# Optimization experiments

Hardware: AMD Instinct MI355X
Metric: run time of the kernel (lower is better)

The kernel has to match this reference:

```python
import jax, jax.numpy as jnp
import numpy as np

INPUT_DIM = 512
LATENT_DIM = 64
H1, H2 = 128, 64  # hardcoded hidden widths in Encoder/Decoder
BATCH = 4096


def _xavier(key, shape):
    fan_out, fan_in = shape
    std = jnp.sqrt(2.0 / (fan_in + fan_out))
    return std * jax.random.normal(key, shape, dtype=jnp.float32)


def setup_inputs() -> dict:
    key = jax.random.key(0)
    ks = jax.random.split(key, 10)
    d = LATENT_DIM
    n_pairs = d * (d - 1) // 2
    n_funcs = 1 + d + n_pairs  # bias + states + pairwise products
    inp = {
        "x": jax.random.normal(ks[0], (BATCH, INPUT_DIM), dtype=jnp.float32),
        "xdot": jax.random.normal(ks[1], (BATCH, INPUT_DIM), dtype=jnp.float32),
        # encoder weights (torch Linear layout: [out, in])
        "We1": _xavier(ks[2], (H1, INPUT_DIM)), "be1": jnp.zeros((H1,), jnp.float32),
        "We2": _xavier(ks[3], (H2, H1)),        "be2": jnp.zeros((H2,), jnp.float32),
        "We3": _xavier(ks[4], (d, H2)),         "be3": jnp.zeros((d,), jnp.float32),
        # decoder weights
        "Wd1": _xavier(ks[5], (H2, d)),         "bd1": jnp.zeros((H2,), jnp.float32),
        "Wd2": _xavier(ks[6], (H1, H2)),        "bd2": jnp.zeros((H1,), jnp.float32),
        "Wd3": _xavier(ks[7], (INPUT_DIM, H1)), "bd3": jnp.zeros((INPUT_DIM,), jnp.float32),
        "XI": jnp.ones((n_funcs, d), jnp.float32),
        "XI_mask": jnp.ones((n_funcs, d), jnp.float32),
    }
    return inp


def _mlp_with_jacobian(x, Ws, bs):
    """3-layer relu MLP; returns output and per-sample analytic Jacobian [B,out,in].
    Jacobian = diag(m3) W3 diag(m2) W2 diag(m1) W1 with relu masks m_l."""
    h = x
    J = None
    for W, b in zip(Ws, bs):
        h = h @ W.T + b                      # [B, out_l]
        m = (h > 0).astype(h.dtype)          # relu mask (grad 0 at 0, matching torch)
        h = jnp.maximum(h, 0)
        Wm = m[:, :, None] * W[None]         # [B, out_l, in_l]
        J = Wm if J is None else jnp.einsum('boh,bhi->boi', Wm, J)
    return h, J


def _sindy_library(z):
    B, d = z.shape
    iu, ju = np.triu_indices(d, k=1)
    ones = jnp.ones((B, 1), z.dtype)
    pairs = z[:, iu] * z[:, ju]              # [B, d(d-1)/2]
    return jnp.concatenate([ones, z, pairs], axis=1)


def reference(x, xdot, We1, be1, We2, be2, We3, be3,
              Wd1, bd1, Wd2, bd2, Wd3, bd3, XI, XI_mask):
    z, Jenc = _mlp_with_jacobian(x, (We1, We2, We3), (be1, be2, be3))
    dz_dt = jnp.einsum('bli,bi->bl', Jenc, xdot)
    xh, Jdec = _mlp_with_jacobian(z, (Wd1, Wd2, Wd3), (bd1, bd2, bd3))
    theta = _sindy_library(z)
    dz_dt_sindy = theta @ (XI_mask * XI)
    dxh_dt = jnp.einsum('bol,bl->bo', Jdec, dz_dt_sindy)
    return (xh, dxh_dt, z, dz_dt, dz_dt_sindy)
```

## Files before the change

kernel.cpp:

```cpp
#include <hip/hip_runtime.h>

#define BATCH 4096
#define IN_DIM 512
#define H1DIM 128
#define H2DIM 64
#define DDIM 64
#define NFUNC 2081
#define NFPAD 2112
#define CHUNK 704
#define KS_PER_CHUNK 22

typedef short bf16x8 __attribute__((ext_vector_type(8)));
typedef float f32x4 __attribute__((ext_vector_type(4)));
#define MFMA(a,b,c) __builtin_amdgcn_mfma_f32_16x16x32_bf16(a,b,c,0,0,0)

#define WSZ1 (H1DIM*IN_DIM)
#define WSZ2 (H2DIM*H1DIM)
#define WSZ3 (DDIM*H2DIM)
#define WSZ4 (H2DIM*DDIM)
#define WSZ5 (H1DIM*H2DIM)
#define WSZ6 (IN_DIM*H1DIM)

__device__ __forceinline__ short f2b(float f) {
    union { float f; unsigned u; } x; x.f = f;
    unsigned r = x.u + 0x7fffu + ((x.u >> 16) & 1u);
    return (short)(r >> 16);
}
__device__ __forceinline__ float b2f(short s) {
    union { unsigned u; float f; } x; x.u = ((unsigned)(unsigned short)s) << 16;
    return x.f;
}
__device__ __forceinline__ void split3f(float v, short& s0, short& s1, short& s2) {
    s0 = f2b(v); float r = v - b2f(s0);
    s1 = f2b(r); float r2 = r - b2f(s1);
    s2 = f2b(r2);
}
__device__ __forceinline__ uint2 pk4(const short* s) {
    union { short s[4]; uint2 u; } z;
    z.s[0] = s[0]; z.s[1] = s[1]; z.s[2] = s[2]; z.s[3] = s[3];
    return z.u;
}

__device__ __forceinline__ void st_b16(short* t, int RS, int r, int c, short v) {
    int b = (c * 2) ^ ((r & 7) << 4);
    *(short*)((char*)(t + r * RS) + b) = v;
}
__device__ __forceinline__ void st_b64(short* t, int RS, int r, int c0, uint2 v) {
    int b = (c0 * 2) ^ ((r & 7) << 4);
    *(uint2*)((char*)(t + r * RS) + b) = v;
}
__device__ __forceinline__ bf16x8 ld_af(const short* t, int RS, int lane, int kbase) {
    int r = lane & 15;
    int b = ((kbase + (lane >> 4) * 8) * 2) ^ ((r & 7) << 4);
    return *(const bf16x8*)((const char*)(t + r * RS) + b);
}
__device__ __forceinline__ bf16x8 ld_bp(const short* P, int blk, int lane) {
    return *(const bf16x8*)(P + ((size_t)blk * 64 + lane) * 8);
}

__device__ __forceinline__ void mf9(bf16x8 f0, bf16x8 f1, bf16x8 f2, bf16x8 fv,
                                    bf16x8 b0, bf16x8 b1, bf16x8 b2,
                                    f32x4& P, f32x4& Q, f32x4& V) {
    P = MFMA(f0, b0, P); Q = MFMA(f1, b1, Q);
    P = MFMA(f1, b0, P); Q = MFMA(f0, b1, Q);
    P = MFMA(f2, b0, P); Q = MFMA(f2, b1, Q);
    P = MFMA(f0, b2, P); Q = MFMA(f1, b2, Q);
    V = MFMA(fv, b0, V);
}

__device__ __forceinline__ void epi_store(short* t0, short* t1, short* t2, short* tv, int RS,
                                          int lane, int col, const f32x4& P, const f32x4& Q,
                                          const f32x4& V, float bb)
{
    #pragma unroll
    for (int q = 0; q < 4; ++q) {
        int row = (lane >> 4) * 4 + q;
        float pre = P[q] + Q[q] + bb;
        float h = fmaxf(pre, 0.f);
        short s0, s1, s2;
        split3f(h, s0, s1, s2);
        st_b16(t0, RS, row, col, s0);
        st_b16(t1, RS, row, col, s1);
        st_b16(t2, RS, row, col, s2);
        st_b16(tv, RS, row, col, pre > 0.f ? f2b(V[q]) : (short)0);
    }
}

template<int K>
__device__ void pack_w(const float* __restrict__ W, short* __restrict__ dst, int NK,
                       int gid, int nthr)
{
    for (int i = gid; i < NK; i += nthr) {
        int c = i / K, k = i % K;
        int cb = c >> 4, ks = k >> 5;
        int L = (((k >> 3) & 3) << 4) | (c & 15);
        int j = k & 7;
        int idx = ((cb * (K / 32) + ks) * 64 + L) * 8 + j;
        short s0, s1, s2; split3f(W[i], s0, s1, s2);
        dst[idx] = s0; dst[idx + NK] = s1; dst[idx + 2 * NK] = s2;
    }
}

__global__ void initk(const float* __restrict__ x, const float* __restrict__ xdot,
                      const float* __restrict__ We1, const float* __restrict__ We2,
                      const float* __restrict__ We3, const float* __restrict__ Wd1,
                      const float* __restrict__ Wd2, const float* __restrict__ Wd3,
                      const float* __restrict__ XI, const float* __restrict__ XIm,
                      float* __restrict__ xh, float* __restrict__ dxh,
                      short* Wp1, short* Wp2, short* Wp3, short* Wp4, short* Wp5, short* Wp6,
                      short* xiP, int2* pk)
{
    int gid = blockIdx.x * blockDim.x + threadIdx.x;
    int nthr = gridDim.x * blockDim.x;

    for (int i = gid; i < (BATCH / 16) * 16 * 64; i += nthr) {
        int L = i & 63, ks = (i >> 6) & 15, rb = i >> 10;
        int row = rb * 16 + (L & 15);
        int k0 = ks * 32 + ((L >> 4) << 3);
        const float* px = &x[(size_t)row * IN_DIM + k0];
        const float* pd = &xdot[(size_t)row * IN_DIM + k0];
        union { short s[8]; bf16x8 v; } a0, a1, a2, dv;
        #pragma unroll
        for (int j = 0; j < 8; ++j) {
            split3f(px[j], a0.s[j], a1.s[j], a2.s[j]);
            dv.s[j] = f2b(pd[j]);
        }
        short* bx = (short*)(xh + (size_t)rb * 8192);
        short* bd = (short*)(dxh + (size_t)rb * 8192);
        int off = (ks * 64 + L) * 8;
        *(bf16x8*)(bx + off) = a0.v;
        *(bf16x8*)(bx + 8192 + off) = a1.v;
        *(bf16x8*)(bd + off) = a2.v;
        *(bf16x8*)(bd + 8192 + off) = dv.v;
    }

    pack_w<512>(We1, Wp1, WSZ1, gid, nthr);
    pack_w<128>(We2, Wp2, WSZ2, gid, nthr);
    pack_w<64>(We3, Wp3, WSZ3, gid, nthr);
    pack_w<64>(Wd1, Wp4, WSZ4, gid, nthr);
    pack_w<64>(Wd2, Wp5, WSZ5, gid, nthr);
    pack_w<128>(Wd3, Wp6, WSZ6, gid, nthr);

    for (int i = gid; i < 4 * 66 * 64; i += nthr) {
        int cb = i / (66 * 64);
        int r = i - cb * (66 * 64);
        int ks = r >> 6, L = r & 63;
        int col = cb * 16 + (L & 15);
        union { short s[8]; bf16x8 v; } w;
        #pragma unroll
        for (int j = 0; j < 8; ++j) {
            int f = ks * 32 + ((L >> 4) << 3) + j;
            float v = (f < NFUNC) ? XI[(size_t)f * DDIM + col] * XIm[(size_t)f * DDIM + col] : 0.f;
            w.s[j] = f2b(v);
        }
        *(bf16x8*)(xiP + (size_t)i * 8) = w.v;
    }

    for (int f = gid; f < NFPAD; f += nthr) {
        int a, b;
        if (f == 0) { a = 64; b = 64; }
        else if (f <= DDIM) { a = f - 1; b = 64; }
        else if (f < NFUNC) {
            int p = f - 1 - DDIM; int i2 = 0, cum = 0;
            while (cum + (63 - i2) <= p) { cum += 63 - i2; ++i2; }
            a = i2; b = i2 + 1 + (p - cum);
        } else { a = 65; b = 65; }
        pk[f] = make_int2(a, b);
    }
}

__global__ __launch_bounds__(256, 1)
void fused(const float* __restrict__ be1, const float* __restrict__ be2,
           const float* __restrict__ be3, const float* __restrict__ bd1,
           const float* __restrict__ bd2, const float* __restrict__ bd3,
           const short* __restrict__ Wp1, const short* __restrict__ Wp2,
           const short* __restrict__ Wp3, const short* __restrict__ Wp4,
           const short* __restrict__ Wp5, const short* __restrict__ Wp6,
           const short* __restrict__ xiP, const int2* __restrict__ pk,
           float* __restrict__ xh, float* __restrict__ dxh, float* __restrict__ zo,
           float* __restrict__ dz, float* __restrict__ dzs)
{
    __shared__ __align__(16) char ldsbuf[37120];
    short* h1s0 = (short*)(ldsbuf + 0);
    short* h1s1 = (short*)(ldsbuf + 4096);
    short* h1s2 = (short*)(ldsbuf + 8192);
    short* v1   = (short*)(ldsbuf + 12288);
    short* h2s0 = (short*)(ldsbuf + 16384);
    short* h2s1 = (short*)(ldsbuf + 18432);
    short* h2s2 = (short*)(ldsbuf + 20480);
    short* v2   = (short*)(ldsbuf + 22528);
    short* th   = (short*)(ldsbuf + 0);
    short* g1s0 = (short*)(ldsbuf + 0);
    short* g1s1 = (short*)(ldsbuf + 2048);
    short* g1s2 = (short*)(ldsbuf + 4096);
    short* u1   = (short*)(ldsbuf + 6144);
    short* g2s0 = (short*)(ldsbuf + 8192);
    short* g2s1 = (short*)(ldsbuf + 12288);
    short* g2s2 = (short*)(ldsbuf + 16384);
    short* u2   = (short*)(ldsbuf + 20480);
    short* zb0  = (short*)(ldsbuf + 24576);
    short* zb1  = (short*)(ldsbuf + 26624);
    short* zb2  = (short*)(ldsbuf + 28672);
    short* dzsb = (short*)(ldsbuf + 30720);
    float* zf   = (float*)(ldsbuf + 32768);

    const int tid = threadIdx.x, lane = tid & 63, wave = tid >> 6;
    const int row0 = blockIdx.x * 16;
    const int c16 = lane & 15;

    float bb1[2] = { be1[wave * 32 + c16], be1[wave * 32 + 16 + c16] };
    float bb2 = be2[wave * 16 + c16];
    float bb3 = be3[wave * 16 + c16];
    float bD1 = bd1[wave * 16 + c16];
    float bD2[2] = { bd2[wave * 32 + c16], bd2[wave * 32 + 16 + c16] };
    float bD3[8];
    #pragma unroll
    for (int i = 0; i < 8; ++i) bD3[i] = bd3[wave * 128 + i * 16 + c16];

    bf16x8 L2B[4][3];

    {
        const short* bx = (const short*)(xh + (size_t)blockIdx.x * 8192);
        const short* bd = (const short*)(dxh + (size_t)blockIdx.x * 8192);
        f32x4 P[2] = {}, Q[2] = {}, V[2] = {};
        bf16x8 A0[3], A1[3], A2[3], Ad[3];
        bf16x8 B0[3][2], B1[3][2], B2[3][2];
#define L1_LA(ks, sl) { int off = ((ks) * 64 + lane) * 8; \
        A0[sl] = *(const bf16x8*)(bx + off); A1[sl] = *(const bf16x8*)(bx + 8192 + off); \
        A2[sl] = *(const bf16x8*)(bd + off); Ad[sl] = *(const bf16x8*)(bd + 8192 + off); }
#define L1_LB(ks, sl) { int bA = (wave * 2) * 16 + (ks), bB = (wave * 2 + 1) * 16 + (ks); \
        B0[sl][0] = ld_bp(Wp1, bA, lane); B1[sl][0] = ld_bp(Wp1 + WSZ1, bA, lane); B2[sl][0] = ld_bp(Wp1 + 2 * WSZ1, bA, lane); \
        B0[sl][1] = ld_bp(Wp1, bB, lane); B1[sl][1] = ld_bp(Wp1 + WSZ1, bB, lane); B2[sl][1] = ld_bp(Wp1 + 2 * WSZ1, bB, lane); }
        L1_LA(0, 0) L1_LB(0, 0)
        L1_LA(1, 1) L1_LB(1, 1)
        L1_LA(2, 2) L1_LB(2, 2)
        #pragma unroll
        for (int ks = 0; ks < 16; ++ks) {
            const int sl = ks % 3;
            mf9(A0[sl], A1[sl], A2[sl], Ad[sl], B0[sl][0], B1[sl][0], B2[sl][0], P[0], Q[0], V[0]);
            mf9(A0[sl], A1[sl], A2[sl], Ad[sl], B0[sl][1], B1[sl][1], B2[sl][1], P[1], Q[1], V[1]);
            if (ks + 3 < 16) { L1_LA(ks + 3, sl) L1_LB(ks + 3, sl) }
        }
#undef L1_LA
#undef L1_LB
        #pragma unroll
        for (int nf = 0; nf < 2; ++nf) {
            int col = wave * 32 + nf * 16 + c16;
            epi_store(h1s0, h1s1, h1s2, v1, 128, lane, col, P[nf], Q[nf], V[nf], bb1[nf]);
        }
        #pragma unroll
        for (int ks = 0; ks < 4; ++ks) {
            int blk = wave * 4 + ks;
            L2B[ks][0] = ld_bp(Wp2, blk, lane);
            L2B[ks][1] = ld_bp(Wp2 + WSZ2, blk, lane);
            L2B[ks][2] = ld_bp(Wp2 + 2 * WSZ2, blk, lane);
        }
    }
    __syncthreads();

    bf16x8 L3B[2][3];
    {
        bf16x8 Aa[4][4];
        #pragma unroll
        for (int ks = 0; ks < 4; ++ks) {
            Aa[ks][0] = ld_af(h1s0, 128, lane, ks * 32);
            Aa[ks][1] = ld_af(h1s1, 128, lane, ks * 32);
            Aa[ks][2] = ld_af(h1s2, 128, lane, ks * 32);
            Aa[ks][3] = ld_af(v1, 128, lane, ks * 32);
        }
        f32x4 P = {}, Q = {}, V = {};
        #pragma unroll
        for (int ks = 0; ks < 4; ++ks)
            mf9(Aa[ks][0], Aa[ks][1], Aa[ks][2], Aa[ks][3], L2B[ks][0], L2B[ks][1], L2B[ks][2], P, Q, V);
        epi_store(h2s0, h2s1, h2s2, v2, 64, lane, wave * 16 + c16, P, Q, V, bb2);
        #pragma unroll
        for (int ks = 0; ks < 2; ++ks) {
            int blk = wave * 2 + ks;
            L3B[ks][0] = ld_bp(Wp3, blk, lane);
            L3B[ks][1] = ld_bp(Wp3 + WSZ3, blk, lane);
            L3B[ks][2] = ld_bp(Wp3 + 2 * WSZ3, blk, lane);
        }
    }
    __syncthreads();

    {
        bf16x8 Aa[2][4];
        #pragma unroll
        for (int ks = 0; ks < 2; ++ks) {
            Aa[ks][0] = ld_af(h2s0, 64, lane, ks * 32);
            Aa[ks][1] = ld_af(h2s1, 64, lane, ks * 32);
            Aa[ks][2] = ld_af(h2s2, 64, lane, ks * 32);
            Aa[ks][3] = ld_af(v2, 64, lane, ks * 32);
        }
        f32x4 P = {}, Q = {}, V = {};
        #pragma unroll
        for (int ks = 0; ks < 2; ++ks)
            mf9(Aa[ks][0], Aa[ks][1], Aa[ks][2], Aa[ks][3], L3B[ks][0], L3B[ks][1], L3B[ks][2], P, Q, V);
        int col = wave * 16 + c16;
        #pragma unroll
        for (int q = 0; q < 4; ++q) {
            int row = (lane >> 4) * 4 + q;
            float pre = P[q] + Q[q] + bb3;
            float hz = fmaxf(pre, 0.f);
            float vz = pre > 0.f ? V[q] : 0.f;
            zf[row * 68 + col] = hz;
            short s0, s1, s2;
            split3f(hz, s0, s1, s2);
            st_b16(zb0, 64, row, col, s0);
            st_b16(zb1, 64, row, col, s1);
            st_b16(zb2, 64, row, col, s2);
            zo[(size_t)(row0 + row) * DDIM + col] = hz;
            dz[(size_t)(row0 + row) * DDIM + col] = vz;
        }
        if (tid < 32) { int r = tid & 15; zf[r * 68 + 64 + (tid >> 4)] = (tid >> 4) ? 0.f : 1.f; }
    }
    __syncthreads();

    {
        f32x4 sa0 = {}, sa1 = {};
        const int tr = tid & 15, tf44 = (tid >> 4) * 44;
        bf16x8 X[KS_PER_CHUNK];
        #pragma unroll
        for (int kk = 0; kk < KS_PER_CHUNK; ++kk)
            X[kk] = ld_bp(xiP, wave * 66 + kk, lane);
        #pragma unroll
        for (int ch = 0; ch < 3; ++ch) {
            #pragma unroll
            for (int g = 0; g < 11; ++g) {
                int fl = tf44 + g * 4;
                int fg = ch * CHUNK + fl;
                int4 qa = *(const int4*)&pk[fg];
                int4 qb = *(const int4*)&pk[fg + 2];
                float t0 = zf[tr * 68 + qa.x] * zf[tr * 68 + qa.y];
                float t1 = zf[tr * 68 + qa.z] * zf[tr * 68 + qa.w];
                float t2 = zf[tr * 68 + qb.x] * zf[tr * 68 + qb.y];
                float t3 = zf[tr * 68 + qb.z] * zf[tr * 68 + qb.w];
                short arr[4] = { f2b(t0), f2b(t1), f2b(t2), f2b(t3) };
                st_b64(th, 704, tr, fl, pk4(arr));
            }
            __syncthreads();
            #pragma unroll
            for (int kk = 0; kk < KS_PER_CHUNK; ++kk) {
                bf16x8 a = ld_af(th, 704, lane, kk * 32);
                if (kk & 1) sa1 = MFMA(a, X[kk], sa1);
                else        sa0 = MFMA(a, X[kk], sa0);
            }
            if (ch < 2) {
                #pragma unroll
                for (int kk = 0; kk < KS_PER_CHUNK; ++kk)
                    X[kk] = ld_bp(xiP, wave * 66 + (ch + 1) * KS_PER_CHUNK + kk, lane);
            }
            __syncthreads();
        }
        f32x4 sacc = sa0 + sa1;
        int col = wave * 16 + c16;
        #pragma unroll
        for (int q = 0; q < 4; ++q) {
            int row = (lane >> 4) * 4 + q;
            float v = sacc[q];
            dzs[(size_t)(row0 + row) * DDIM + col] = v;
            st_b16(dzsb, 64, row, col, f2b(v));
        }
    }
    bf16x8 D1B[2][3];
    #pragma unroll
    for (int ks = 0; ks < 2; ++ks) {
        int blk = wave * 2 + ks;
        D1B[ks][0] = ld_bp(Wp4, blk, lane);
        D1B[ks][1] = ld_bp(Wp4 + WSZ4, blk, lane);
        D1B[ks][2] = ld_bp(Wp4 + 2 * WSZ4, blk, lane);
    }
    __syncthreads();

    bf16x8 D2B[2][2][3];
    {
        bf16x8 Aa[2][4];
        #pragma unroll
        for (int ks = 0; ks < 2; ++ks) {
            Aa[ks][0] = ld_af(zb0, 64, lane, ks * 32);
            Aa[ks][1] = ld_af(zb1, 64, lane, ks * 32);
            Aa[ks][2] = ld_af(zb2, 64, lane, ks * 32);
            Aa[ks][3] = ld_af(dzsb, 64, lane, ks * 32);
        }
        f32x4 P = {}, Q = {}, V = {};
        #pragma unroll
        for (int ks = 0; ks < 2; ++ks)
            mf9(Aa[ks][0], Aa[ks][1], Aa[ks][2], Aa[ks][3], D1B[ks][0], D1B[ks][1], D1B[ks][2], P, Q, V);
        epi_store(g1s0, g1s1, g1s2, u1, 64, lane, wave * 16 + c16, P, Q, V, bD1);
        #pragma unroll
        for (int cf = 0; cf < 2; ++cf)
            #pragma unroll
            for (int ks = 0; ks < 2; ++ks) {
                int blk = (wave * 2 + cf) * 2 + ks;
                D2B[cf][ks][0] = ld_bp(Wp5, blk, lane);
                D2B[cf][ks][1] = ld_bp(Wp5 + WSZ5, blk, lane);
                D2B[cf][ks][2] = ld_bp(Wp5 + 2 * WSZ5, blk, lane);
            }
    }
    __syncthreads();

    {
        bf16x8 Aa[2][4];
        #pragma unroll
        for (int ks = 0; ks < 2; ++ks) {
            Aa[ks][0] = ld_af(g1s0, 64, lane, ks * 32);
            Aa[ks][1] = ld_af(g1s1, 64, lane, ks * 32);
            Aa[ks][2] = ld_af(g1s2, 64, lane, ks * 32);
            Aa[ks][3] = ld_af(u1, 64, lane, ks * 32);
        }
        f32x4 P[2] = {}, Q[2] = {}, V[2] = {};
        #pragma unroll
        for (int cf = 0; cf < 2; ++cf)
            #pragma unroll
            for (int ks = 0; ks < 2; ++ks)
                mf9(Aa[ks][0], Aa[ks][1], Aa[ks][2], Aa[ks][3],
                    D2B[cf][ks][0], D2B[cf][ks][1], D2B[cf][ks][2], P[cf], Q[cf], V[cf]);
        #pragma unroll
        for (int cf = 0; cf < 2; ++cf) {
            int col = wave * 32 + cf * 16 + c16;
            epi_store(g2s0, g2s1, g2s2, u2, 128, lane, col, P[cf], Q[cf], V[cf], bD2[cf]);
        }
    }
    __syncthreads();

    #pragma unroll
    for (int h = 0; h < 2; ++h) {
        f32x4 P[4] = {}, Q[4] = {}, V[4] = {};
        bf16x8 Bp[4][3];
        bf16x8 Ax0[2], Ax1[2], Ax2[2], Axv[2];
#define D3_LA(ks, b) { Ax0[b] = ld_af(g2s0, 128, lane, (ks) * 32); Ax1[b] = ld_af(g2s1, 128, lane, (ks) * 32); \
                       Ax2[b] = ld_af(g2s2, 128, lane, (ks) * 32); Axv[b] = ld_af(u2, 128, lane, (ks) * 32); }
#define D3_LB(s, sl) { int blk = (wave * 8 + h * 4 + ((s) & 3)) * 4 + ((s) >> 2); \
        Bp[sl][0] = ld_bp(Wp6, blk, lane); Bp[sl][1] = ld_bp(Wp6 + WSZ6, blk, lane); Bp[sl][2] = ld_bp(Wp6 + 2 * WSZ6, blk, lane); }
        D3_LA(0, 0)
        D3_LB(0, 0) D3_LB(1, 1) D3_LB(2, 2) D3_LB(3, 3)
        #pragma unroll
        for (int ks = 0; ks < 4; ++ks) {
            if (ks < 3) D3_LA(ks + 1, (ks + 1) & 1)
            #pragma unroll
            for (int cf = 0; cf < 4; ++cf) {
                const int s = ks * 4 + cf, sl = s & 3;
                mf9(Ax0[ks & 1], Ax1[ks & 1], Ax2[ks & 1], Axv[ks & 1],
                    Bp[sl][0], Bp[sl][1], Bp[sl][2], P[cf], Q[cf], V[cf]);
                if (s + 4 < 16) D3_LB(s + 4, sl)
            }
        }
#undef D3_LA
#undef D3_LB
        #pragma unroll
        for (int cf = 0; cf < 4; ++cf) {
            int col = wave * 128 + h * 64 + cf * 16 + c16;
            float bb = bD3[h * 4 + cf];
            #pragma unroll
            for (int q = 0; q < 4; ++q) {
                int row = (lane >> 4) * 4 + q;
                float pre = P[cf][q] + Q[cf][q] + bb;
                xh[(size_t)(row0 + row) * IN_DIM + col] = fmaxf(pre, 0.f);
                dxh[(size_t)(row0 + row) * IN_DIM + col] = pre > 0.f ? V[cf][q] : 0.f;
            }
        }
    }
}

extern "C" void kernel_launch(void* const* d_in, const int* in_sizes, int n_in,
                              void* d_out, int out_size, void* d_ws, size_t ws_size,
                              hipStream_t stream)
{
    const float* x    = (const float*)d_in[0];
    const float* xdot = (const float*)d_in[1];
    const float* We1  = (const float*)d_in[2];
    const float* be1  = (const float*)d_in[3];
    const float* We2  = (const float*)d_in[4];
    const float* be2  = (const float*)d_in[5];
    const float* We3  = (const float*)d_in[6];
    const float* be3  = (const float*)d_in[7];
    const float* Wd1  = (const float*)d_in[8];
    const float* bd1  = (const float*)d_in[9];
    const float* Wd2  = (const float*)d_in[10];
    const float* bd2  = (const float*)d_in[11];
    const float* Wd3  = (const float*)d_in[12];
    const float* bd3  = (const float*)d_in[13];
    const float* XI   = (const float*)d_in[14];
    const float* XIm  = (const float*)d_in[15];

    float* out = (float*)d_out;
    float* xh  = out;
    float* dxh = out + (size_t)BATCH * IN_DIM;
    float* zo  = dxh + (size_t)BATCH * IN_DIM;
    float* dz  = zo + (size_t)BATCH * DDIM;
    float* dzs = dz + (size_t)BATCH * DDIM;

    int2*  pk  = (int2*)d_ws;
    short* Wp1 = (short*)(pk + NFPAD);
    short* Wp2 = Wp1 + 3 * WSZ1;
    short* Wp3 = Wp2 + 3 * WSZ2;
    short* Wp4 = Wp3 + 3 * WSZ3;
    short* Wp5 = Wp4 + 3 * WSZ4;
    short* Wp6 = Wp5 + 3 * WSZ5;
    short* xiP = Wp6 + 3 * WSZ6;

    initk<<<1024, 256, 0, stream>>>(x, xdot, We1, We2, We3, Wd1, Wd2, Wd3, XI, XIm,
                                    xh, dxh, Wp1, Wp2, Wp3, Wp4, Wp5, Wp6, xiP, pk);
    fused<<<BATCH / 16, 256, 0, stream>>>(be1, be2, be3, bd1, bd2, bd3,
                                          Wp1, Wp2, Wp3, Wp4, Wp5, Wp6, xiP, pk,
                                          xh, dxh, zo, dz, dzs);
}
```

Baseline: 51.31 us.

## Double fused kernel block to 512 threads and vectorize init packing

The fused kernel now launches 8 waves per 16-row block instead of 4, with launch bounds of 512 threads and 2 blocks per CU. Layer 1, decoder layer 2 and the output layer split their columns across all 8 waves. The narrow 64-wide layers and the SINDy MFMA run only on waves 0-3, while all threads build the library tile. The init kernel now uses vector float4 loads of x/xdot and packs weights eight values at a time with 16-byte stores. This trades more parallelism and occupancy for idle waves in the narrow stages and extra barriers.

```diff
diff --git a/kernel.cpp b/kernel.cpp
--- a/kernel.cpp
+++ b/kernel.cpp
@@ -35,19 +35,14 @@
     s1 = f2b(r); float r2 = r - b2f(s1);
     s2 = f2b(r2);
 }
-__device__ __forceinline__ uint2 pk4(const short* s) {
-    union { short s[4]; uint2 u; } z;
-    z.s[0] = s[0]; z.s[1] = s[1]; z.s[2] = s[2]; z.s[3] = s[3];
-    return z.u;
-}
 
 __device__ __forceinline__ void st_b16(short* t, int RS, int r, int c, short v) {
     int b = (c * 2) ^ ((r & 7) << 4);
     *(short*)((char*)(t + r * RS) + b) = v;
 }
-__device__ __forceinline__ void st_b64(short* t, int RS, int r, int c0, uint2 v) {
-    int b = (c0 * 2) ^ ((r & 7) << 4);
-    *(uint2*)((char*)(t + r * RS) + b) = v;
+__device__ __forceinline__ void st_b32s(short* t, int RS, int r, int c, unsigned v) {
+    int b = (c * 2) ^ ((r & 7) << 4);
+    *(unsigned*)((char*)(t + r * RS) + b) = v;
 }
 __device__ __forceinline__ bf16x8 ld_af(const short* t, int RS, int lane, int kbase) {
     int r = lane & 15;
@@ -90,14 +85,18 @@
 __device__ void pack_w(const float* __restrict__ W, short* __restrict__ dst, int NK,
                        int gid, int nthr)
 {
-    for (int i = gid; i < NK; i += nthr) {
-        int c = i / K, k = i % K;
-        int cb = c >> 4, ks = k >> 5;
-        int L = (((k >> 3) & 3) << 4) | (c & 15);
-        int j = k & 7;
-        int idx = ((cb * (K / 32) + ks) * 64 + L) * 8 + j;
-        short s0, s1, s2; split3f(W[i], s0, s1, s2);
-        dst[idx] = s0; dst[idx + NK] = s1; dst[idx + 2 * NK] = s2;
+    for (int o = gid; o < NK / 8; o += nthr) {
+        int c = o / (K / 8), k0 = (o - c * (K / 8)) * 8;
+        int cb = c >> 4, ks = k0 >> 5;
+        int L = (((k0 >> 3) & 3) << 4) | (c & 15);
+        int idx = ((cb * (K / 32) + ks) * 64 + L) * 8;
+        union { short s[8]; bf16x8 v; } p0, p1, p2;
+        #pragma unroll
+        for (int j = 0; j < 8; ++j)
+            split3f(W[(size_t)c * K + k0 + j], p0.s[j], p1.s[j], p2.s[j]);
+        *(bf16x8*)(dst + idx) = p0.v;
+        *(bf16x8*)(dst + NK + idx) = p1.v;
+        *(bf16x8*)(dst + 2 * NK + idx) = p2.v;
     }
 }
 
@@ -119,11 +118,14 @@
         int k0 = ks * 32 + ((L >> 4) << 3);
         const float* px = &x[(size_t)row * IN_DIM + k0];
         const float* pd = &xdot[(size_t)row * IN_DIM + k0];
+        f32x4 xa = *(const f32x4*)px, xb = *(const f32x4*)(px + 4);
+        f32x4 da = *(const f32x4*)pd, db = *(const f32x4*)(pd + 4);
         union { short s[8]; bf16x8 v; } a0, a1, a2, dv;
         #pragma unroll
-        for (int j = 0; j < 8; ++j) {
-            split3f(px[j], a0.s[j], a1.s[j], a2.s[j]);
-            dv.s[j] = f2b(pd[j]);
+        for (int j = 0; j < 4; ++j) {
+            split3f(xa[j], a0.s[j], a1.s[j], a2.s[j]);
+            split3f(xb[j], a0.s[j + 4], a1.s[j + 4], a2.s[j + 4]);
+            dv.s[j] = f2b(da[j]); dv.s[j + 4] = f2b(db[j]);
         }
         short* bx = (short*)(xh + (size_t)rb * 8192);
         short* bd = (short*)(dxh + (size_t)rb * 8192);
@@ -169,7 +171,7 @@
     }
 }
 
-__global__ __launch_bounds__(256, 1)
+__global__ __launch_bounds__(512, 2)
 void fused(const float* __restrict__ be1, const float* __restrict__ be2,
            const float* __restrict__ be3, const float* __restrict__ bd1,
            const float* __restrict__ bd2, const float* __restrict__ bd3,
@@ -205,52 +207,50 @@
     float* zf   = (float*)(ldsbuf + 32768);
 
     const int tid = threadIdx.x, lane = tid & 63, wave = tid >> 6;
+    const int wq = wave & 3;
     const int row0 = blockIdx.x * 16;
     const int c16 = lane & 15;
-
-    float bb1[2] = { be1[wave * 32 + c16], be1[wave * 32 + 16 + c16] };
-    float bb2 = be2[wave * 16 + c16];
-    float bb3 = be3[wave * 16 + c16];
-    float bD1 = bd1[wave * 16 + c16];
-    float bD2[2] = { bd2[wave * 32 + c16], bd2[wave * 32 + 16 + c16] };
-    float bD3[8];
+    const int tr = tid & 15, bg = tid >> 4;
+    const int tf = bg * 22;
+
+    float bb1 = be1[wave * 16 + c16];
+    float bb2 = be2[wq * 16 + c16];
+    float bb3 = be3[wq * 16 + c16];
+    float bD1 = bd1[wq * 16 + c16];
+    float bD2 = bd2[wave * 16 + c16];
+    float bD3[4];
     #pragma unroll
-    for (int i = 0; i < 8; ++i) bD3[i] = bd3[wave * 128 + i * 16 + c16];
-
-    bf16x8 L2B[4][3];
+    for (int i = 0; i < 4; ++i) bD3[i] = bd3[wave * 64 + i * 16 + c16];
 
     {
         const short* bx = (const short*)(xh + (size_t)blockIdx.x * 8192);
         const short* bd = (const short*)(dxh + (size_t)blockIdx.x * 8192);
-        f32x4 P[2] = {}, Q[2] = {}, V[2] = {};
-        bf16x8 A0[3], A1[3], A2[3], Ad[3];
-        bf16x8 B0[3][2], B1[3][2], B2[3][2];
+        f32x4 P = {}, Q = {}, V = {};
+        bf16x8 A0[3], A1[3], A2[3], Ad[3], B0[3], B1[3], B2[3];
 #define L1_LA(ks, sl) { int off = ((ks) * 64 + lane) * 8; \
         A0[sl] = *(const bf16x8*)(bx + off); A1[sl] = *(const bf16x8*)(bx + 8192 + off); \
         A2[sl] = *(const bf16x8*)(bd + off); Ad[sl] = *(const bf16x8*)(bd + 8192 + off); }
-#define L1_LB(ks, sl) { int bA = (wave * 2) * 16 + (ks), bB = (wave * 2 + 1) * 16 + (ks); \
-        B0[sl][0] = ld_bp(Wp1, bA, lane); B1[sl][0] = ld_bp(Wp1 + WSZ1, bA, lane); B2[sl][0] = ld_bp(Wp1 + 2 * WSZ1, bA, lane); \
-        B0[sl][1] = ld_bp(Wp1, bB, lane); B1[sl][1] = ld_bp(Wp1 + WSZ1, bB, lane); B2[sl][1] = ld_bp(Wp1 + 2 * WSZ1, bB, lane); }
+#define L1_LB(ks, sl) { int blk = wave * 16 + (ks); \
+        B0[sl] = ld_bp(Wp1, blk, lane); B1[sl] = ld_bp(Wp1 + WSZ1, blk, lane); \
+        B2[sl] = ld_bp(Wp1 + 2 * WSZ1, blk, lane); }
         L1_LA(0, 0) L1_LB(0, 0)
         L1_LA(1, 1) L1_LB(1, 1)
         L1_LA(2, 2) L1_LB(2, 2)
         #pragma unroll
         for (int ks = 0; ks < 16; ++ks) {
             const int sl = ks % 3;
-            mf9(A0[sl], A1[sl], A2[sl], Ad[sl], B0[sl][0], B1[sl][0], B2[sl][0], P[0], Q[0], V[0]);
-            mf9(A0[sl], A1[sl], A2[sl], Ad[sl], B0[sl][1], B1[sl][1], B2[sl][1], P[1], Q[1], V[1]);
+            mf9(A0[sl], A1[sl], A2[sl], Ad[sl], B0[sl], B1[sl], B2[sl], P, Q, V);
             if (ks + 3 < 16) { L1_LA(ks + 3, sl) L1_LB(ks + 3, sl) }
         }
 #undef L1_LA
 #undef L1_LB
-        #pragma unroll
-        for (int nf = 0; nf < 2; ++nf) {
-            int col = wave * 32 + nf * 16 + c16;
-            epi_store(h1s0, h1s1, h1s2, v1, 128, lane, col, P[nf], Q[nf], V[nf], bb1[nf]);
-        }
+        epi_store(h1s0, h1s1, h1s2, v1, 128, lane, wave * 16 + c16, P, Q, V, bb1);
+    }
+    bf16x8 L2B[4][3];
+    if (wave < 4) {
         #pragma unroll
         for (int ks = 0; ks < 4; ++ks) {
-            int blk = wave * 4 + ks;
+            int blk = wq * 4 + ks;
             L2B[ks][0] = ld_bp(Wp2, blk, lane);
             L2B[ks][1] = ld_bp(Wp2 + WSZ2, blk, lane);
             L2B[ks][2] = ld_bp(Wp2 + 2 * WSZ2, blk, lane);
@@ -259,7 +259,7 @@
     __syncthreads();
 
     bf16x8 L3B[2][3];
-    {
+    if (wave < 4) {
         bf16x8 Aa[4][4];
         #pragma unroll
         for (int ks = 0; ks < 4; ++ks) {
@@ -268,22 +268,23 @@
             Aa[ks][2] = ld_af(h1s2, 128, lane, ks * 32);
             Aa[ks][3] = ld_af(v1, 128, lane, ks * 32);
         }
-        f32x4 P = {}, Q = {}, V = {};
-        #pragma unroll
-        for (int ks = 0; ks < 4; ++ks)
-            mf9(Aa[ks][0], Aa[ks][1], Aa[ks][2], Aa[ks][3], L2B[ks][0], L2B[ks][1], L2B[ks][2], P, Q, V);
-        epi_store(h2s0, h2s1, h2s2, v2, 64, lane, wave * 16 + c16, P, Q, V, bb2);
         #pragma unroll
         for (int ks = 0; ks < 2; ++ks) {
-            int blk = wave * 2 + ks;
+            int blk = wq * 2 + ks;
             L3B[ks][0] = ld_bp(Wp3, blk, lane);
             L3B[ks][1] = ld_bp(Wp3 + WSZ3, blk, lane);
             L3B[ks][2] = ld_bp(Wp3 + 2 * WSZ3, blk, lane);
         }
-    }
-    __syncthreads();
-
-    {
+        f32x4 P = {}, Q = {}, V = {};
+        #pragma unroll
+        for (int ks = 0; ks < 4; ++ks)
+            mf9(Aa[ks][0], Aa[ks][1], Aa[ks][2], Aa[ks][3], L2B[ks][0], L2B[ks][1], L2B[ks][2], P, Q, V);
+        epi_store(h2s0, h2s1, h2s2, v2, 64, lane, wq * 16 + c16, P, Q, V, bb2);
+    }
+    __syncthreads();
+
+    bf16x8 X[KS_PER_CHUNK];
+    if (wave < 4) {
         bf16x8 Aa[2][4];
         #pragma unroll
         for (int ks = 0; ks < 2; ++ks) {
@@ -296,7 +297,10 @@
         #pragma unroll
         for (int ks = 0; ks < 2; ++ks)
             mf9(Aa[ks][0], Aa[ks][1], Aa[ks][2], Aa[ks][3], L3B[ks][0], L3B[ks][1], L3B[ks][2], P, Q, V);
-        int col = wave * 16 + c16;
+        #pragma unroll
+        for (int kk = 0; kk < KS_PER_CHUNK; ++kk)
+            X[kk] = ld_bp(xiP, wq * 66 + kk, lane);
+        int col = wq * 16 + c16;
         #pragma unroll
         for (int q = 0; q < 4; ++q) {
             int row = (lane >> 4) * 4 + q;
@@ -316,44 +320,47 @@
     }
     __syncthreads();
 
-    {
-        f32x4 sa0 = {}, sa1 = {};
-        const int tr = tid & 15, tf44 = (tid >> 4) * 44;
-        bf16x8 X[KS_PER_CHUNK];
-        #pragma unroll
-        for (int kk = 0; kk < KS_PER_CHUNK; ++kk)
-            X[kk] = ld_bp(xiP, wave * 66 + kk, lane);
-        #pragma unroll
-        for (int ch = 0; ch < 3; ++ch) {
-            #pragma unroll
-            for (int g = 0; g < 11; ++g) {
-                int fl = tf44 + g * 4;
-                int fg = ch * CHUNK + fl;
-                int4 qa = *(const int4*)&pk[fg];
-                int4 qb = *(const int4*)&pk[fg + 2];
-                float t0 = zf[tr * 68 + qa.x] * zf[tr * 68 + qa.y];
-                float t1 = zf[tr * 68 + qa.z] * zf[tr * 68 + qa.w];
-                float t2 = zf[tr * 68 + qb.x] * zf[tr * 68 + qb.y];
-                float t3 = zf[tr * 68 + qb.z] * zf[tr * 68 + qb.w];
-                short arr[4] = { f2b(t0), f2b(t1), f2b(t2), f2b(t3) };
-                st_b64(th, 704, tr, fl, pk4(arr));
-            }
-            __syncthreads();
-            #pragma unroll
-            for (int kk = 0; kk < KS_PER_CHUNK; ++kk) {
-                bf16x8 a = ld_af(th, 704, lane, kk * 32);
-                if (kk & 1) sa1 = MFMA(a, X[kk], sa1);
-                else        sa0 = MFMA(a, X[kk], sa0);
-            }
-            if (ch < 2) {
-                #pragma unroll
-                for (int kk = 0; kk < KS_PER_CHUNK; ++kk)
-                    X[kk] = ld_bp(xiP, wave * 66 + (ch + 1) * KS_PER_CHUNK + kk, lane);
-            }
-            __syncthreads();
-        }
+    f32x4 sa0 = {}, sa1 = {};
+    auto build = [&](int ch) {
+        #pragma clang loop unroll(disable)
+        for (int j = 0; j < 11; ++j) {
+            int f0 = ch * CHUNK + tf + 2 * j;
+            int2 p0 = pk[f0], p1 = pk[f0 + 1];
+            float t0 = zf[tr * 68 + p0.x] * zf[tr * 68 + p0.y];
+            float t1 = zf[tr * 68 + p1.x] * zf[tr * 68 + p1.y];
+            unsigned u = (unsigned)(unsigned short)f2b(t0)
+                       | ((unsigned)(unsigned short)f2b(t1) << 16);
+            st_b32s(th, 704, tr, tf + 2 * j, u);
+        }
+    };
+#define SMF() { _Pragma("unroll") for (int kk = 0; kk < KS_PER_CHUNK; ++kk) { \
+        bf16x8 a = ld_af(th, 704, lane, kk * 32); \
+        if (kk & 1) sa1 = MFMA(a, X[kk], sa1); else sa0 = MFMA(a, X[kk], sa0); } }
+#define ISX(ch) { _Pragma("unroll") for (int kk = 0; kk < KS_PER_CHUNK; ++kk) \
+        X[kk] = ld_bp(xiP, wq * 66 + (ch) * KS_PER_CHUNK + kk, lane); }
+
+    build(0);
+    __syncthreads();
+    if (wave < 4) { SMF() ISX(1) }
+    __syncthreads();
+    build(1);
+    __syncthreads();
+    if (wave < 4) { SMF() ISX(2) }
+    __syncthreads();
+    build(2);
+    __syncthreads();
+    bf16x8 D1B[2][3];
+    if (wave < 4) {
+        SMF()
         f32x4 sacc = sa0 + sa1;
-        int col = wave * 16 + c16;
+        #pragma unroll
+        for (int ks = 0; ks < 2; ++ks) {
+            int blk = wq * 2 + ks;
+            D1B[ks][0] = ld_bp(Wp4, blk, lane);
+            D1B[ks][1] = ld_bp(Wp4 + WSZ4, blk, lane);
+            D1B[ks][2] = ld_bp(Wp4 + 2 * WSZ4, blk, lane);
+        }
+        int col = wq * 16 + c16;
         #pragma unroll
         for (int q = 0; q < 4; ++q) {
             int row = (lane >> 4) * 4 + q;
@@ -362,18 +369,12 @@
             st_b16(dzsb, 64, row, col, f2b(v));
         }
     }
-    bf16x8 D1B[2][3];
-    #pragma unroll
-    for (int ks = 0; ks < 2; ++ks) {
-        int blk = wave * 2 + ks;
-        D1B[ks][0] = ld_bp(Wp4, blk, lane);
-        D1B[ks][1] = ld_bp(Wp4 + WSZ4, blk, lane);
-        D1B[ks][2] = ld_bp(Wp4 + 2 * WSZ4, blk, lane);
-    }
-    __syncthreads();
-
-    bf16x8 D2B[2][2][3];
-    {
+#undef SMF
+#undef ISX
+    __syncthreads();
+
+    bf16x8 D2B[2][3];
+    if (wave < 4) {
         bf16x8 Aa[2][4];
         #pragma unroll
         for (int ks = 0; ks < 2; ++ks) {
@@ -386,16 +387,14 @@
         #pragma unroll
         for (int ks = 0; ks < 2; ++ks)
             mf9(Aa[ks][0], Aa[ks][1], Aa[ks][2], Aa[ks][3], D1B[ks][0], D1B[ks][1], D1B[ks][2], P, Q, V);
-        epi_store(g1s0, g1s1, g1s2, u1, 64, lane, wave * 16 + c16, P, Q, V, bD1);
-        #pragma unroll
-        for (int cf = 0; cf < 2; ++cf)
-            #pragma unroll
-            for (int ks = 0; ks < 2; ++ks) {
-                int blk = (wave * 2 + cf) * 2 + ks;
-                D2B[cf][ks][0] = ld_bp(Wp5, blk, lane);
-                D2B[cf][ks][1] = ld_bp(Wp5 + WSZ5, blk, lane);
-                D2B[cf][ks][2] = ld_bp(Wp5 + 2 * WSZ5, blk, lane);
-            }
+        epi_store(g1s0, g1s1, g1s2, u1, 64, lane, wq * 16 + c16, P, Q, V, bD1);
+    }
+    #pragma unroll
+    for (int ks = 0; ks < 2; ++ks) {
+        int blk = wave * 2 + ks;
+        D2B[ks][0] = ld_bp(Wp5, blk, lane);
+        D2B[ks][1] = ld_bp(Wp5 + WSZ5, blk, lane);
+        D2B[ks][2] = ld_bp(Wp5 + 2 * WSZ5, blk, lane);
     }
     __syncthreads();
 
@@ -408,30 +407,23 @@
             Aa[ks][2] = ld_af(g1s2, 64, lane, ks * 32);
             Aa[ks][3] = ld_af(u1, 64, lane, ks * 32);
         }
-        f32x4 P[2] = {}, Q[2] = {}, V[2] = {};
-        #pragma unroll
-        for (int cf = 0; cf < 2; ++cf)
-            #pragma unroll
-            for (int ks = 0; ks < 2; ++ks)
-                mf9(Aa[ks][0], Aa[ks][1], Aa[ks][2], Aa[ks][3],
-                    D2B[cf][ks][0], D2B[cf][ks][1], D2B[cf][ks][2], P[cf], Q[cf], V[cf]);
-        #pragma unroll
-        for (int cf = 0; cf < 2; ++cf) {
-            int col = wave * 32 + cf * 16 + c16;
-            epi_store(g2s0, g2s1, g2s2, u2, 128, lane, col, P[cf], Q[cf], V[cf], bD2[cf]);
-        }
-    }
-    __syncthreads();
-
-    #pragma unroll
-    for (int h = 0; h < 2; ++h) {
+        f32x4 P = {}, Q = {}, V = {};
+        #pragma unroll
+        for (int ks = 0; ks < 2; ++ks)
+            mf9(Aa[ks][0], Aa[ks][1], Aa[ks][2], Aa[ks][3], D2B[ks][0], D2B[ks][1], D2B[ks][2], P, Q, V);
+        epi_store(g2s0, g2s1, g2s2, u2, 128, lane, wave * 16 + c16, P, Q, V, bD2);
+    }
+    __syncthreads();
+
+    {
         f32x4 P[4] = {}, Q[4] = {}, V[4] = {};
         bf16x8 Bp[4][3];
         bf16x8 Ax0[2], Ax1[2], Ax2[2], Axv[2];
 #define D3_LA(ks, b) { Ax0[b] = ld_af(g2s0, 128, lane, (ks) * 32); Ax1[b] = ld_af(g2s1, 128, lane, (ks) * 32); \
                        Ax2[b] = ld_af(g2s2, 128, lane, (ks) * 32); Axv[b] = ld_af(u2, 128, lane, (ks) * 32); }
-#define D3_LB(s, sl) { int blk = (wave * 8 + h * 4 + ((s) & 3)) * 4 + ((s) >> 2); \
-        Bp[sl][0] = ld_bp(Wp6, blk, lane); Bp[sl][1] = ld_bp(Wp6 + WSZ6, blk, lane); Bp[sl][2] = ld_bp(Wp6 + 2 * WSZ6, blk, lane); }
+#define D3_LB(s, sl) { int blk = (wave * 4 + ((s) & 3)) * 4 + ((s) >> 2); \
+        Bp[sl][0] = ld_bp(Wp6, blk, lane); Bp[sl][1] = ld_bp(Wp6 + WSZ6, blk, lane); \
+        Bp[sl][2] = ld_bp(Wp6 + 2 * WSZ6, blk, lane); }
         D3_LA(0, 0)
         D3_LB(0, 0) D3_LB(1, 1) D3_LB(2, 2) D3_LB(3, 3)
         #pragma unroll
@@ -449,8 +441,8 @@
 #undef D3_LB
         #pragma unroll
         for (int cf = 0; cf < 4; ++cf) {
-            int col = wave * 128 + h * 64 + cf * 16 + c16;
-            float bb = bD3[h * 4 + cf];
+            int col = wave * 64 + cf * 16 + c16;
+            float bb = bD3[cf];
             #pragma unroll
             for (int q = 0; q < 4; ++q) {
                 int row = (lane >> 4) * 4 + q;
@@ -501,7 +493,7 @@
 
     initk<<<1024, 256, 0, stream>>>(x, xdot, We1, We2, We3, Wd1, Wd2, Wd3, XI, XIm,
                                     xh, dxh, Wp1, Wp2, Wp3, Wp4, Wp5, Wp6, xiP, pk);
-    fused<<<BATCH / 16, 256, 0, stream>>>(be1, be2, be3, bd1, bd2, bd3,
+    fused<<<BATCH / 16, 512, 0, stream>>>(be1, be2, be3, bd1, bd2, bd3,
                                           Wp1, Wp2, Wp3, Wp4, Wp5, Wp6, xiP, pk,
                                           xh, dxh, zo, dz, dzs);
 }
```

Result: faster. 50.19 us (-2.2%).
